# Kernel optimization log

Hardware: AMD Instinct MI355X
Metric: run time of the kernel (lower is better)

## Reference

```python
import jax, jax.numpy as jnp
import numpy as np

B, T, D, M = 4, 4096, 2048, 512


def setup_inputs() -> dict:
    key = jax.random.key(0)
    ks = jax.random.split(key, 6)
    x = jax.random.normal(ks[0], (B, T, D), dtype=jnp.float32)
    memory_state = jnp.zeros((B, M), dtype=jnp.float32)
    # xavier_normal-style init for the linear layers, zero biases
    Wv = jax.random.normal(ks[1], (M, D), dtype=jnp.float32) * np.float32(np.sqrt(2.0 / (D + M)))
    bv = jnp.zeros((M,), dtype=jnp.float32)
    Wg = jax.random.normal(ks[2], (D, D + M), dtype=jnp.float32) * np.float32(np.sqrt(2.0 / (2 * D + M)))
    bg = jnp.zeros((D,), dtype=jnp.float32)
    time_decay = jax.random.normal(ks[3], (M,), dtype=jnp.float32) * 0.01
    time_first = jax.random.normal(ks[4], (M,), dtype=jnp.float32) * 0.01
    return dict(x=x, memory_state=memory_state, Wv=Wv, bv=bv, Wg=Wg, bg=bg,
                time_decay=time_decay, time_first=time_first)


def reference(x, memory_state, Wv, bv, Wg, bg, time_decay, time_first):
    # v = value_proj(x): [B, T, M]
    v = jnp.einsum('btd,md->btm', x, Wv) + bv
    decay = jax.nn.sigmoid(time_decay) * 0.9 + 0.1   # [M]
    first = jax.nn.sigmoid(time_first)               # [M]

    # Recurrence: s_0 = memory_state; wv_t = v_t + s_t*first; s_{t+1} = s_t*decay + v_t
    def step(s, v_t):
        wv_t = v_t + s * first
        return s * decay + v_t, wv_t

    v_tb = jnp.swapaxes(v, 0, 1)                     # [T, B, M] for scan over time
    next_memory, wv_tb = jax.lax.scan(step, memory_state, v_tb)
    weighted_values = jnp.swapaxes(wv_tb, 0, 1)      # [B, T, M]

    # output = x + output_gate(concat[x, weighted_values])
    combined = jnp.concatenate([x, weighted_values], axis=-1)  # [B, T, D+M]
    output = x + jnp.einsum('btk,dk->btd', combined, Wg) + bg
    return output, next_memory
```

## Files before the change

### kernel.cpp

```cpp
#include <hip/hip_runtime.h>
#include <hip/hip_bf16.h>
#include <cstdint>
#include <cstddef>

#define B_DIM 4
#define T_DIM 4096
#define D_DIM 2048
#define M_DIM 512
#define NTOK  (B_DIM * T_DIM)
#define KCOMB (D_DIM + M_DIM)
#define NCHUNK 64
#define CLEN   64

typedef __attribute__((ext_vector_type(8)))  __bf16 bf16x8;
typedef __attribute__((ext_vector_type(16))) float  f32x16;

__device__ __forceinline__ unsigned short f2bf(float f) {
  union { float f; unsigned u; } v; v.f = f;
  unsigned r = v.u + 0x7fffu + ((v.u >> 16) & 1u);
  return (unsigned short)(r >> 16);
}

__device__ __forceinline__ float sigmoidf(float x) { return 1.0f / (1.0f + expf(-x)); }

#define XBLK  ((NTOK * D_DIM / 4) / 256)
#define WVBLK ((M_DIM * D_DIM / 4) / 256)
#define WGBLK ((D_DIM * KCOMB / 4) / 256)
__global__ void cast_all_kernel(const float* __restrict__ x, const float* __restrict__ Wv,
                                const float* __restrict__ Wg,
                                unsigned short* __restrict__ comb,
                                unsigned short* __restrict__ WvB,
                                unsigned short* __restrict__ WgB) {
  int bid = blockIdx.x;
  const float* src; unsigned short* dst; size_t soff, doff;
  if (bid < XBLK) {
    int idx = bid * 256 + threadIdx.x;
    int n = idx >> 9;
    int c = (idx & 511) << 2;
    src = x;   soff = (size_t)n * D_DIM + c;
    dst = comb; doff = (size_t)n * KCOMB + c;
  } else if (bid < XBLK + WVBLK) {
    int idx = (bid - XBLK) * 256 + threadIdx.x;
    src = Wv;  soff = (size_t)idx * 4;
    dst = WvB; doff = (size_t)idx * 4;
  } else {
    int idx = (bid - XBLK - WVBLK) * 256 + threadIdx.x;
    src = Wg;  soff = (size_t)idx * 4;
    dst = WgB; doff = (size_t)idx * 4;
  }
  float4 v = *(const float4*)(src + soff);
  ushort4 o;
  o.x = f2bf(v.x); o.y = f2bf(v.y); o.z = f2bf(v.z); o.w = f2bf(v.w);
  *(ushort4*)(dst + doff) = o;
}

__global__ __launch_bounds__(M_DIM) void recur_partial(
    const float* __restrict__ v, const float* __restrict__ td, float* __restrict__ P) {
  int m = threadIdx.x;
  int b = blockIdx.x >> 6;
  int c = blockIdx.x & (NCHUNK - 1);
  float decay = sigmoidf(td[m]) * 0.9f + 0.1f;
  const float* vp = v + ((size_t)(b * T_DIM + c * CLEN)) * M_DIM + m;
  float p = 0.0f;
  for (int t0 = 0; t0 < CLEN; t0 += 8) {
    float vt[8];
#pragma unroll
    for (int u = 0; u < 8; ++u) vt[u] = vp[(size_t)(t0 + u) * M_DIM];
#pragma unroll
    for (int u = 0; u < 8; ++u) p = p * decay + vt[u];
  }
  P[(size_t)blockIdx.x * M_DIM + m] = p;
}

__global__ __launch_bounds__(M_DIM) void recur_apply(
    const float* __restrict__ v, const float* __restrict__ mem0,
    const float* __restrict__ td, const float* __restrict__ tf,
    const float* __restrict__ P,
    unsigned short* __restrict__ comb, float* __restrict__ nmem) {
  int m = threadIdx.x;
  int b = blockIdx.x >> 6;
  int c = blockIdx.x & (NCHUNK - 1);
  float decay = sigmoidf(td[m]) * 0.9f + 0.1f;
  float first = sigmoidf(tf[m]);
  float dL = decay;
  dL = dL * dL; dL = dL * dL; dL = dL * dL; dL = dL * dL; dL = dL * dL; dL = dL * dL;

  float s = mem0[b * M_DIM + m];
  const float* Pp = P + (size_t)(b * NCHUNK) * M_DIM + m;
  for (int ci = 0; ci < c; ++ci)
    s = s * dL + Pp[(size_t)ci * M_DIM];

  const float* vp = v + ((size_t)(b * T_DIM + c * CLEN)) * M_DIM + m;
  unsigned short* wp = comb + ((size_t)(b * T_DIM + c * CLEN)) * KCOMB + D_DIM + m;
  for (int t0 = 0; t0 < CLEN; t0 += 8) {
    float vt[8];
#pragma unroll
    for (int u = 0; u < 8; ++u) vt[u] = vp[(size_t)(t0 + u) * M_DIM];
#pragma unroll
    for (int u = 0; u < 8; ++u) {
      wp[(size_t)(t0 + u) * KCOMB] = f2bf(vt[u] + s * first);
      s = s * decay + vt[u];
    }
  }
  if (c == NCHUNK - 1) nmem[b * M_DIM + m] = s;
}

#define BM 128
#define BN 128
#define BK 64

template <bool ADD_X, int MODE>
__global__ __launch_bounds__(256) void gemm_bt(
    const unsigned short* __restrict__ A, int lda,
    const unsigned short* __restrict__ B, int ldb,
    const float* __restrict__ bias, const float* __restrict__ xadd,
    float* __restrict__ C, int N, int K) {
  const int tid = threadIdx.x;
  const int lane = tid & 63;
  const int wave = tid >> 6;
  const int wm = (wave >> 1) * 64;
  const int wn = (wave & 1) * 64;
  const int l31 = lane & 31;
  const int half = lane >> 5;

  int tileM, tileN;
  {
    int idx = blockIdx.x;
    int xcd = idx & 7, local = idx >> 3;
    if (MODE == 1) {
      tileN = (xcd * 2 + (local & 1)) * BN;
      tileM = (local >> 1) * BM;
    } else {
      tileM = (xcd * 16 + (local >> 2)) * BM;
      tileN = (local & 3) * BN;
    }
  }

  __shared__ unsigned short As[BM * BK];
  __shared__ unsigned short Bs[BN * BK];

  f32x16 acc[2][2] = {};

  for (int k0 = 0; k0 < K; k0 += BK) {
#pragma unroll
    for (int j = 0; j < 4; ++j) {
      int c = j * 256 + tid;
      int row = c >> 3;
      int kc = c & 7;
      int gkc = kc ^ (row & 7);
      const unsigned short* gA = A + (size_t)(tileM + row) * lda + k0 + gkc * 8;
      const unsigned short* gB = B + (size_t)(tileN + row) * ldb + k0 + gkc * 8;
      __builtin_amdgcn_global_load_lds((const __attribute__((address_space(1))) void*)gA,
                                       (__attribute__((address_space(3))) void*)(As + c * 8),
                                       16, 0, 0);
      __builtin_amdgcn_global_load_lds((const __attribute__((address_space(1))) void*)gB,
                                       (__attribute__((address_space(3))) void*)(Bs + c * 8),
                                       16, 0, 0);
    }
    __syncthreads();

#pragma unroll
    for (int s = 0; s < 4; ++s) {
      const int g = s * 2 + half;
      bf16x8 af[2], bfr[2];
#pragma unroll
      for (int i = 0; i < 2; ++i) {
        int ra = wm + i * 32 + l31;
        int rb = wn + i * 32 + l31;
        af[i]  = *(const bf16x8*)(As + ra * BK + ((g ^ (ra & 7)) * 8));
        bfr[i] = *(const bf16x8*)(Bs + rb * BK + ((g ^ (rb & 7)) * 8));
      }
#pragma unroll
      for (int mi = 0; mi < 2; ++mi)
#pragma unroll
        for (int ni = 0; ni < 2; ++ni)
          acc[mi][ni] = __builtin_amdgcn_mfma_f32_32x32x16_bf16(af[mi], bfr[ni], acc[mi][ni], 0, 0, 0);
    }
    __syncthreads();
  }

#pragma unroll
  for (int mi = 0; mi < 2; ++mi) {
#pragma unroll
    for (int ni = 0; ni < 2; ++ni) {
      int col = tileN + wn + ni * 32 + l31;
      float bcol = bias[col];
#pragma unroll
      for (int r = 0; r < 16; ++r) {
        int row = tileM + wm + mi * 32 + 4 * half + (r & 3) + 8 * (r >> 2);
        float val = acc[mi][ni][r] + bcol;
        if (ADD_X) val += xadd[(size_t)row * N + col];
        C[(size_t)row * N + col] = val;
      }
    }
  }
}

extern "C" void kernel_launch(void* const* d_in, const int* in_sizes, int n_in,
                              void* d_out, int out_size, void* d_ws, size_t ws_size,
                              hipStream_t stream) {
  const float* x   = (const float*)d_in[0];
  const float* mem = (const float*)d_in[1];
  const float* Wv  = (const float*)d_in[2];
  const float* bv  = (const float*)d_in[3];
  const float* Wg  = (const float*)d_in[4];
  const float* bg  = (const float*)d_in[5];
  const float* td  = (const float*)d_in[6];
  const float* tf  = (const float*)d_in[7];
  float* out = (float*)d_out;

  char* ws = (char*)d_ws;
  unsigned short* comb = (unsigned short*)ws;
  float* v = (float*)(ws + (size_t)NTOK * KCOMB * 2);
  unsigned short* WvB = (unsigned short*)((char*)v + (size_t)NTOK * M_DIM * 4);
  unsigned short* WgB = (unsigned short*)((char*)WvB + (size_t)M_DIM * D_DIM * 2);
  float* P = (float*)WvB;

  cast_all_kernel<<<XBLK + WVBLK + WGBLK, 256, 0, stream>>>(x, Wv, Wg, comb, WvB, WgB);

  gemm_bt<false, 0><<<(NTOK / BM) * (M_DIM / BN), 256, 0, stream>>>(
      comb, KCOMB, WvB, D_DIM, bv, nullptr, v, M_DIM, D_DIM);

  recur_partial<<<B_DIM * NCHUNK, M_DIM, 0, stream>>>(v, td, P);
  recur_apply<<<B_DIM * NCHUNK, M_DIM, 0, stream>>>(
      v, mem, td, tf, P, comb, out + (size_t)NTOK * D_DIM);

  gemm_bt<true, 1><<<(NTOK / BM) * (D_DIM / BN), 256, 0, stream>>>(
      comb, KCOMB, WgB, KCOMB, bg, x, out, D_DIM, KCOMB);
}
```

Baseline: 531.2 us.

## Replace output-gate GEMM with 256x256 double-buffered pipelined MFMA kernel

Adds a new GEMM kernel for the large output-gate projection that uses 256x256 tiles, 512 threads (8 waves), double-buffered LDS and a hand-scheduled 8-phase loop. Global-to-LDS staging is interleaved with MFMA work, ordered by explicit waitcnt and barriers, with raised wave priority during the MFMA bursts. The aim is higher data reuse per tile and overlap of memory loads with compute, which the old single-buffered 128x128 kernel lacked. The cost is heavy LDS use (128 KB) and high register pressure, and the hand-written waitcnt schedule is fragile.

```diff
diff --git a/kernel.cpp b/kernel.cpp
--- a/kernel.cpp
+++ b/kernel.cpp
@@ -196,6 +196,172 @@
   }
 }
 
+#define BAR_FENCE() do { asm volatile("" ::: "memory"); \
+  __builtin_amdgcn_s_barrier(); asm volatile("" ::: "memory"); } while (0)
+
+template <bool ADD_X, int LDA, int LDB, int NOUT, int KTOT>
+__global__ __launch_bounds__(512, 2) void gemm256_bt(
+    const unsigned short* __restrict__ Amat,
+    const unsigned short* __restrict__ Bmat,
+    const float* __restrict__ bias,
+    const float* __restrict__ xadd,
+    float* __restrict__ C) {
+  constexpr int NK  = KTOT / 64;
+  constexpr int NI  = NK / 2;
+  constexpr int NTN = NOUT / 256;
+  constexpr int NWG = (NTOK / 256) * NTN;
+  constexpr int PERX = NWG / 8;
+
+  __shared__ unsigned short As[2][256 * 64];
+  __shared__ unsigned short Bs[2][256 * 64];
+
+  const int tid  = threadIdx.x;
+  const int lane = tid & 63;
+  const int half = lane >> 5;
+  const int l31  = lane & 31;
+  const int wave = tid >> 6;
+  const int wrow = (wave >> 2) * 128;
+  const int wcol = (wave & 3) * 64;
+
+  const int bid   = blockIdx.x;
+  const int wgid  = (bid & 7) * PERX + (bid >> 3);
+  const int tileM = (wgid / NTN) * 256;
+  const int tileN = (wgid % NTN) * 256;
+
+  const int row_lo = tid >> 3;
+  const int scol   = (((tid & 7) ^ (row_lo & 7)) << 3);
+  const unsigned short* pA = Amat + (size_t)(tileM + row_lo) * LDA + scol;
+  const unsigned short* pB = Bmat + (size_t)(tileN + row_lo) * LDB + scol;
+
+#define STAGE_A(b, h, kt) do { \
+  _Pragma("unroll") for (int j = 0; j < 2; ++j) { \
+    const unsigned short* _s = pA + (size_t)((h) * 128 + j * 64) * LDA + (kt) * 64; \
+    __builtin_amdgcn_global_load_lds((const __attribute__((address_space(1))) void*)_s, \
+        (__attribute__((address_space(3))) void*)(&As[(b)][(h) * 8192 + (j * 512 + tid) * 8]), \
+        16, 0, 0); \
+  } \
+} while (0)
+
+#define STAGE_B(b, h, kt) do { \
+  _Pragma("unroll") for (int j = 0; j < 2; ++j) { \
+    const unsigned short* _s = pB + (size_t)((h) * 128 + j * 64) * LDB + (kt) * 64; \
+    __builtin_amdgcn_global_load_lds((const __attribute__((address_space(1))) void*)_s, \
+        (__attribute__((address_space(3))) void*)(&Bs[(b)][(h) * 8192 + (j * 512 + tid) * 8]), \
+        16, 0, 0); \
+  } \
+} while (0)
+
+  f32x16 acc[4][2] = {};
+  bf16x8 af[2][4];
+  bf16x8 bfr[4];
+
+#define READ_A(b, mh) do { \
+  _Pragma("unroll") for (int mi = 0; mi < 2; ++mi) { \
+    const int _r = wrow + (mh) * 64 + mi * 32 + l31; \
+    _Pragma("unroll") for (int s = 0; s < 4; ++s) \
+      af[mi][s] = *(const bf16x8*)(&As[(b)][_r * 64 + (((s * 2 + half) ^ (_r & 7)) << 3)]); \
+  } \
+} while (0)
+
+#define READ_B(b, ni) do { \
+  const int _r = wcol + (ni) * 32 + l31; \
+  _Pragma("unroll") for (int s = 0; s < 4; ++s) \
+    bfr[s] = *(const bf16x8*)(&Bs[(b)][_r * 64 + (((s * 2 + half) ^ (_r & 7)) << 3)]); \
+} while (0)
+
+#define MFMA_QUAD(mh, ni) do { \
+  _Pragma("unroll") for (int s = 0; s < 4; ++s) \
+    _Pragma("unroll") for (int mi = 0; mi < 2; ++mi) \
+      acc[(mh) * 2 + mi][(ni)] = __builtin_amdgcn_mfma_f32_32x32x16_bf16( \
+          af[mi][s], bfr[s], acc[(mh) * 2 + mi][(ni)], 0, 0, 0); \
+} while (0)
+
+#define PHASE_TAIL(mh, ni) do { \
+  BAR_FENCE(); \
+  asm volatile("s_waitcnt lgkmcnt(0)" ::: "memory"); \
+  __builtin_amdgcn_s_setprio(1); \
+  MFMA_QUAD(mh, ni); \
+  __builtin_amdgcn_s_setprio(0); \
+  BAR_FENCE(); \
+} while (0)
+
+  STAGE_A(0, 0, 0);
+  STAGE_A(0, 1, 0);
+  STAGE_B(0, 0, 0);
+  STAGE_B(0, 1, 0);
+  STAGE_A(1, 0, 1);
+  asm volatile("s_waitcnt vmcnt(2)" ::: "memory");
+  BAR_FENCE();
+
+#define ITER8(KE, FULL) do { \
+   \
+  READ_A(0, 0); READ_B(0, 0); \
+  STAGE_A(1, 1, (KE) + 1); \
+  asm volatile("s_waitcnt lgkmcnt(8)" ::: "memory"); \
+  PHASE_TAIL(0, 0); \
+   \
+  READ_B(0, 1); \
+  STAGE_B(1, 0, (KE) + 1); \
+  PHASE_TAIL(0, 1); \
+   \
+  READ_A(0, 1); \
+  STAGE_B(1, 1, (KE) + 1); \
+  PHASE_TAIL(1, 1); \
+   \
+  READ_B(0, 0); \
+  if (FULL) { STAGE_A(0, 0, (KE) + 2); \
+              asm volatile("s_waitcnt vmcnt(2)" ::: "memory"); } \
+  else      { asm volatile("s_waitcnt vmcnt(0)" ::: "memory"); } \
+  PHASE_TAIL(1, 0); \
+   \
+  READ_A(1, 0); READ_B(1, 0); \
+  if (FULL) STAGE_A(0, 1, (KE) + 2); \
+  asm volatile("s_waitcnt lgkmcnt(8)" ::: "memory"); \
+  PHASE_TAIL(0, 0); \
+   \
+  READ_B(1, 1); \
+  if (FULL) STAGE_B(0, 0, (KE) + 2); \
+  PHASE_TAIL(0, 1); \
+   \
+  READ_A(1, 1); \
+  if (FULL) STAGE_B(0, 1, (KE) + 2); \
+  PHASE_TAIL(1, 1); \
+   \
+  READ_B(1, 0); \
+  if (FULL) { STAGE_A(1, 0, (KE) + 3); \
+              asm volatile("s_waitcnt vmcnt(2)" ::: "memory"); } \
+  PHASE_TAIL(1, 0); \
+} while (0)
+
+#pragma unroll 1
+  for (int i = 0; i < NI - 1; ++i) ITER8(2 * i, 1);
+  ITER8(2 * (NI - 1), 0);
+
+#undef ITER8
+#undef PHASE_TAIL
+#undef MFMA_QUAD
+#undef READ_B
+#undef READ_A
+#undef STAGE_B
+#undef STAGE_A
+
+#pragma unroll
+  for (int mq = 0; mq < 4; ++mq) {
+#pragma unroll
+    for (int ni = 0; ni < 2; ++ni) {
+      const int col = tileN + wcol + ni * 32 + l31;
+      const float bc = bias[col];
+#pragma unroll
+      for (int r = 0; r < 16; ++r) {
+        const int row = tileM + wrow + mq * 32 + 4 * half + (r & 3) + 8 * (r >> 2);
+        float val = acc[mq][ni][r] + bc;
+        if (ADD_X) val += xadd[(size_t)row * NOUT + col];
+        C[(size_t)row * NOUT + col] = val;
+      }
+    }
+  }
+}
+
 extern "C" void kernel_launch(void* const* d_in, const int* in_sizes, int n_in,
                               void* d_out, int out_size, void* d_ws, size_t ws_size,
                               hipStream_t stream) {
@@ -225,6 +391,6 @@
   recur_apply<<<B_DIM * NCHUNK, M_DIM, 0, stream>>>(
       v, mem, td, tf, P, comb, out + (size_t)NTOK * D_DIM);
 
-  gemm_bt<true, 1><<<(NTOK / BM) * (D_DIM / BN), 256, 0, stream>>>(
-      comb, KCOMB, WgB, KCOMB, bg, x, out, D_DIM, KCOMB);
-}
+  gemm256_bt<true, KCOMB, KCOMB, D_DIM, KCOMB>
+      <<<(NTOK / 256) * (D_DIM / 256), 512, 0, stream>>>(comb, WgB, bg, x, out);
+}
```

Result: faster. 512.3 us (-3.6%).
